# Kernel tuning notes

Measured on AMD Instinct MI355X. Metric: run time of the kernel, lower is better.

## Reference

```python
import jax, jax.numpy as jnp
import numpy as np

N_NODES, N_EDGES, HIDDEN, N_GRAPHS = 100000, 500000, 128, 2048
ATOM_DIM, BOND_DIM, OUT_DIM = 4, 3, 1


def setup_inputs() -> dict:
    key = jax.random.key(0)
    ks = jax.random.split(key, 13)
    s = 0.05  # small init scale to keep relu+scatter depth iterations numerically tame
    return {
        "x": jax.random.normal(ks[0], (N_NODES, ATOM_DIM), jnp.float32),
        "edge_index": jax.random.randint(ks[1], (2, N_EDGES), 0, N_NODES, dtype=jnp.int32),
        "edge_attr": jax.random.normal(ks[2], (N_EDGES, BOND_DIM), jnp.float32),
        "batch": jnp.sort(jax.random.randint(ks[3], (N_NODES,), 0, N_GRAPHS, dtype=jnp.int32)),
        "depth": 3,
        # DMPNN weights (bias=False)
        "W_i": jax.random.normal(ks[4], (HIDDEN, ATOM_DIM + BOND_DIM), jnp.float32) * s,
        "W_m": jax.random.normal(ks[5], (HIDDEN, HIDDEN), jnp.float32) * s,
        "W_a": jax.random.normal(ks[6], (HIDDEN, ATOM_DIM + HIDDEN), jnp.float32) * s,
        # FFN: Linear(d,4d) -> relu -> dropout(eval=identity) -> Linear(4d,d)
        "W1": jax.random.normal(ks[7], (4 * HIDDEN, HIDDEN), jnp.float32) * s,
        "b1": jnp.zeros((4 * HIDDEN,), jnp.float32),
        "W2": jax.random.normal(ks[8], (HIDDEN, 4 * HIDDEN), jnp.float32) * s,
        "b2": jnp.zeros((HIDDEN,), jnp.float32),
        "W_last": jax.random.normal(ks[9], (OUT_DIM, HIDDEN), jnp.float32) * s,
        "b_last": jnp.zeros((OUT_DIM,), jnp.float32),
    }


def reference(x, edge_index, edge_attr, batch, depth, W_i, W_m, W_a, W1, b1, W2, b2, W_last, b_last):
    src, dst = edge_index[0], edge_index[1]
    E = edge_attr.shape[0]
    N = x.shape[0]
    # h: per-edge state [E, H]
    h = jax.nn.relu(jnp.concatenate([x[src], edge_attr], axis=1) @ W_i.T)
    for _ in range(depth):
        # message: relu(W_m h) gathered at src, scatter-add to dst; PyG infers
        # dim_size from h (edge-level here), so aggregation buffer has E rows.
        m = jax.nn.relu(h @ W_m.T)
        h = h + jax.ops.segment_sum(m[src], dst, num_segments=E)
    # index_add_ edge states to nodes
    node_emb = jax.ops.segment_sum(h, dst, num_segments=N)  # [N, H]
    node_emb = jax.nn.relu(jnp.concatenate([x, node_emb], axis=1) @ W_a.T)
    # global_add_pool over graphs
    g = jax.ops.segment_sum(node_emb, batch, num_segments=N_GRAPHS)  # [G, H]
    g = jax.nn.relu(g @ W1.T + b1) @ W2.T + b2  # FFN (dropout eval = identity)
    return g @ W_last.T + b_last  # [G, OUT_DIM]
```

## Files before the change

kernel.cpp:

```cpp
#include <hip/hip_runtime.h>


#define NN 100000
#define NE 500000
#define HID 128
#define NG 2048
#define NB_SCAN 391
#define NBLK128 782

typedef __attribute__((ext_vector_type(8))) short bf16x8;
typedef __attribute__((ext_vector_type(4))) float f32x4;

__device__ __forceinline__ float b2f(ushort u) {
  return __uint_as_float(((uint)u) << 16);
}
__device__ __forceinline__ ushort f2b(float f) {
  uint u = __float_as_uint(f);
  return (ushort)((u + 0x7FFF + ((u >> 16) & 1)) >> 16);
}
__device__ __forceinline__ void acc8(float* a, bf16x8 v) {
#pragma unroll
  for (int j = 0; j < 8; ++j) a[j] += b2f((ushort)v[j]);
}
__device__ __forceinline__ bf16x8 pack8(const float* a) {
  bf16x8 o;
#pragma unroll
  for (int j = 0; j < 8; ++j) o[j] = (short)f2b(a[j]);
  return o;
}
__device__ __forceinline__ size_t taddr(int n, int c8) {
  return ((size_t)(c8 >> 4) * NN + n) * 16 + (c8 & 8);
}

__global__ __launch_bounds__(256) void k_convw(const float* __restrict__ Wm,
    const float* __restrict__ Wa, ushort* __restrict__ wmb, ushort* __restrict__ wab) {
  int i = blockIdx.x * 256 + threadIdx.x;
  if (i >= HID * HID) return;
  wmb[i] = f2b(Wm[i]);
  int c = i >> 7, k = i & 127;
  wab[i] = f2b(Wa[c * 132 + 4 + k]);
}

__global__ __launch_bounds__(256) void k_init_h8(const int* __restrict__ src,
    const float* __restrict__ x, const float* __restrict__ ea,
    const float* __restrict__ Wi, ushort* __restrict__ hT) {
  __shared__ float wis[HID * 7];
  for (int i = threadIdx.x; i < HID * 7; i += 256) wis[i] = Wi[i];
  __syncthreads();
  int idx = blockIdx.x * 256 + threadIdx.x;
  int e = idx >> 4, chunk = idx & 15;
  if (e >= NN) return;
  int s = src[e];
  float4 xv = *reinterpret_cast<const float4*>(&x[(size_t)s * 4]);
  float e0 = ea[(size_t)e*3+0], e1 = ea[(size_t)e*3+1], e2 = ea[(size_t)e*3+2];
  const float* w = &wis[chunk * 56];
  float a[8];
#pragma unroll
  for (int j = 0; j < 8; ++j) {
    const float* wj = &w[j * 7];
    float t = xv.x*wj[0] + xv.y*wj[1] + xv.z*wj[2] + xv.w*wj[3]
            + e0*wj[4] + e1*wj[5] + e2*wj[6];
    a[j] = fmaxf(t, 0.f);
  }
  *reinterpret_cast<bf16x8*>(&hT[((size_t)(chunk >> 1) * NN + e) * 16 + (chunk & 1) * 8]) = pack8(a);
}

__global__ __launch_bounds__(256) void k_hist2(const int* __restrict__ dst,
    int* __restrict__ cnt, int* __restrict__ cnt_lo) {
  int e = blockIdx.x * 256 + threadIdx.x;
  if (e >= NE) return;
  int d = dst[e];
  atomicAdd(&cnt[d], 1);
  if (e < NN) atomicAdd(&cnt_lo[d], 1);
}

__global__ __launch_bounds__(256) void k_scan1(const int* __restrict__ cnt,
    int* __restrict__ outp, int* __restrict__ bsums) {
  __shared__ int s[256];
  int t = threadIdx.x;
  int i = blockIdx.x * 256 + t;
  int v = (i < NN) ? cnt[i] : 0;
  s[t] = v;
  __syncthreads();
  for (int off = 1; off < 256; off <<= 1) {
    int u = (t >= off) ? s[t - off] : 0;
    __syncthreads();
    s[t] += u;
    __syncthreads();
  }
  if (i < NN) outp[i] = s[t] - v;
  if (t == 255) bsums[blockIdx.x] = s[255];
}

__global__ __launch_bounds__(512) void k_scan2(int* __restrict__ bsums) {
  __shared__ int s[512];
  int t = threadIdx.x;
  int v = (t < NB_SCAN) ? bsums[t] : 0;
  s[t] = v;
  __syncthreads();
  for (int off = 1; off < 512; off <<= 1) {
    int u = (t >= off) ? s[t - off] : 0;
    __syncthreads();
    s[t] += u;
    __syncthreads();
  }
  if (t < NB_SCAN) bsums[t] = s[t] - v;
}

__global__ __launch_bounds__(256) void k_scan3(int* __restrict__ outp,
                                               const int* __restrict__ bsums) {
  int i = blockIdx.x * 256 + threadIdx.x;
  if (i < NN) outp[i] += bsums[blockIdx.x];
  if (i == 0) outp[NN] = NE;
}

__global__ __launch_bounds__(256) void k_mid(const int* __restrict__ rowptr,
    const int* __restrict__ cnt_lo, int* __restrict__ midp) {
  int i = blockIdx.x * 256 + threadIdx.x;
  if (i < NN) midp[i] = rowptr[i] + cnt_lo[i];
}

__global__ __launch_bounds__(256) void k_fill2z(const int* __restrict__ src,
    const int* __restrict__ dst, const int* __restrict__ rowptr,
    const int* __restrict__ midp, int* __restrict__ cur_lo,
    int* __restrict__ cur_hi, int* __restrict__ csr_src, int* __restrict__ csr_eid,
    const float* __restrict__ x, const float* __restrict__ ea,
    ushort* __restrict__ zpk) {
  int e = blockIdx.x * 256 + threadIdx.x;
  if (e >= NE) return;
  int d = dst[e];
  int s = src[e];
  int o;
  if (e < NN) {
    o = rowptr[d] + atomicAdd(&cur_lo[d], 1);
    csr_eid[o] = e;
  } else {
    o = midp[d] + atomicAdd(&cur_hi[d], 1);
    float4 xv = *reinterpret_cast<const float4*>(&x[(size_t)s * 4]);
    bf16x8 z;
    z[0] = (short)f2b(xv.x); z[1] = (short)f2b(xv.y);
    z[2] = (short)f2b(xv.z); z[3] = (short)f2b(xv.w);
    z[4] = (short)f2b(ea[(size_t)e*3+0]);
    z[5] = (short)f2b(ea[(size_t)e*3+1]);
    z[6] = (short)f2b(ea[(size_t)e*3+2]);
    z[7] = 0;
    *reinterpret_cast<bf16x8*>(&zpk[(size_t)o * 8]) = z;
  }
  csr_src[o] = s;
}

__global__ __launch_bounds__(256) void k_goff(const int* __restrict__ batch,
                                              int* __restrict__ goff) {
  int g = blockIdx.x * 256 + threadIdx.x;
  if (g > NG) return;
  int lo = 0, hi = NN;
  while (lo < hi) { int mid = (lo + hi) >> 1; if (batch[mid] < g) lo = mid + 1; else hi = mid; }
  goff[g] = lo;
}

template <bool HASX>
__global__ __launch_bounds__(256) void k_mfma(const ushort* __restrict__ A,
    const ushort* __restrict__ Wb, const float* __restrict__ X,
    const float* __restrict__ WaF, ushort* __restrict__ O, int nrows) {
  int tid = threadIdx.x;
  int wave = tid >> 6;
  int lane = tid & 63;
  int wr = wave >> 1, wc = wave & 1;
  int row0 = blockIdx.x * 64 + wr * 32;
  int col0 = wc * 64;
  int l15 = lane & 15, l4 = lane >> 4;

  f32x4 acc[2][4];
#pragma unroll
  for (int mi = 0; mi < 2; ++mi)
#pragma unroll
    for (int ni = 0; ni < 4; ++ni) acc[mi][ni] = (f32x4){0.f, 0.f, 0.f, 0.f};

  if (HASX) {
    float4 wv[4];
#pragma unroll
    for (int ni = 0; ni < 4; ++ni)
      wv[ni] = *reinterpret_cast<const float4*>(&WaF[(size_t)(col0 + ni * 16 + l15) * 132]);
#pragma unroll
    for (int mi = 0; mi < 2; ++mi)
#pragma unroll
      for (int j = 0; j < 4; ++j) {
        int r = row0 + mi * 16 + l4 * 4 + j;
        if (r < nrows) {
          float4 xv = *reinterpret_cast<const float4*>(&X[(size_t)r * 4]);
#pragma unroll
          for (int ni = 0; ni < 4; ++ni)
            acc[mi][ni][j] = xv.x * wv[ni].x + xv.y * wv[ni].y
                           + xv.z * wv[ni].z + xv.w * wv[ni].w;
        }
      }
  }

  const bf16x8 zero8 = {0, 0, 0, 0, 0, 0, 0, 0};
#pragma unroll
  for (int k0 = 0; k0 < HID; k0 += 32) {
    bf16x8 a[2], b[4];
    int c8 = k0 + l4 * 8;
#pragma unroll
    for (int mi = 0; mi < 2; ++mi) {
      int r = row0 + mi * 16 + l15;
      a[mi] = (r < nrows)
            ? *reinterpret_cast<const bf16x8*>(&A[taddr(r, c8)])
            : zero8;
    }
#pragma unroll
    for (int ni = 0; ni < 4; ++ni) {
      int c = col0 + ni * 16 + l15;
      b[ni] = *reinterpret_cast<const bf16x8*>(&Wb[(size_t)c * HID + k0 + l4 * 8]);
    }
#pragma unroll
    for (int mi = 0; mi < 2; ++mi)
#pragma unroll
      for (int ni = 0; ni < 4; ++ni)
        acc[mi][ni] = __builtin_amdgcn_mfma_f32_16x16x32_bf16(a[mi], b[ni], acc[mi][ni], 0, 0, 0);
  }

#pragma unroll
  for (int mi = 0; mi < 2; ++mi)
#pragma unroll
    for (int j = 0; j < 4; ++j) {
      int r = row0 + mi * 16 + l4 * 4 + j;
      if (r >= nrows) continue;
#pragma unroll
      for (int ni = 0; ni < 4; ++ni) {
        int plane = wc * 4 + ni;
        O[((size_t)plane * NN + r) * 16 + l15] = f2b(fmaxf(acc[mi][ni][j], 0.f));
      }
    }
}

__global__ __launch_bounds__(256) void k_gather_x(const ushort* __restrict__ mT,
    const int* __restrict__ rowptr, const int* __restrict__ csr_src,
    ushort* __restrict__ hT) {
  int plane = blockIdx.x & 7;
  int nb = blockIdx.x >> 3;
  int n = nb * 128 + (threadIdx.x >> 1);
  if (n >= NN) return;
  int half8 = (threadIdx.x & 1) * 8;
  size_t pb = (size_t)plane * NN;
  size_t base = (pb + n) * 16 + half8;
  const bf16x8 zero8 = {0, 0, 0, 0, 0, 0, 0, 0};
  float a[8];
  bf16x8 hv = *reinterpret_cast<const bf16x8*>(&hT[base]);
#pragma unroll
  for (int j = 0; j < 8; ++j) a[j] = b2f((ushort)hv[j]);
  int beg = rowptr[n], end = rowptr[n + 1];
  for (int i = beg; i < end; i += 8) {
    bf16x8 v[8];
#pragma unroll
    for (int k = 0; k < 8; ++k) {
      v[k] = zero8;
      if (i + k < end) {
        int s = csr_src[i + k];
        v[k] = *reinterpret_cast<const bf16x8*>(&mT[(pb + s) * 16 + half8]);
      }
    }
#pragma unroll
    for (int k = 0; k < 8; ++k) acc8(a, v[k]);
  }
  *reinterpret_cast<bf16x8*>(&hT[base]) = pack8(a);
}

__global__ __launch_bounds__(256) void k_node_agg_x(const ushort* __restrict__ hT,
    const int* __restrict__ rowptr, const int* __restrict__ midp,
    const int* __restrict__ csr_eid, const ushort* __restrict__ zpk,
    const float* __restrict__ Wi, ushort* __restrict__ neT) {
  int plane = blockIdx.x & 7;
  int nb = blockIdx.x >> 3;
  int n = nb * 128 + (threadIdx.x >> 1);
  if (n >= NN) return;
  int half8 = (threadIdx.x & 1) * 8;
  int c8 = plane * 16 + half8;
  float w[8][7];
#pragma unroll
  for (int j = 0; j < 8; ++j)
#pragma unroll
    for (int k = 0; k < 7; ++k) w[j][k] = Wi[(c8 + j) * 7 + k];
  size_t pb = (size_t)plane * NN;
  int beg = rowptr[n], mid = midp[n], end = rowptr[n + 1];
  const bf16x8 zero8 = {0, 0, 0, 0, 0, 0, 0, 0};
  float a[8];
#pragma unroll
  for (int j = 0; j < 8; ++j) a[j] = 0.f;

  for (int i = beg; i < mid; i += 4) {
    bf16x8 v[4];
#pragma unroll
    for (int k = 0; k < 4; ++k) {
      v[k] = zero8;
      if (i + k < mid) {
        int e = csr_eid[i + k];
        v[k] = *reinterpret_cast<const bf16x8*>(&hT[(pb + e) * 16 + half8]);
      }
    }
#pragma unroll
    for (int k = 0; k < 4; ++k) acc8(a, v[k]);
  }

  for (int i = mid; i < end; i += 4) {
    bf16x8 zv[4];
#pragma unroll
    for (int k = 0; k < 4; ++k) {
      zv[k] = zero8;
      if (i + k < end)
        zv[k] = *reinterpret_cast<const bf16x8*>(&zpk[(size_t)(i + k) * 8]);
    }
#pragma unroll
    for (int k = 0; k < 4; ++k) {
      if (i + k < end) {
        float z0 = b2f((ushort)zv[k][0]), z1 = b2f((ushort)zv[k][1]);
        float z2 = b2f((ushort)zv[k][2]), z3 = b2f((ushort)zv[k][3]);
        float z4 = b2f((ushort)zv[k][4]), z5 = b2f((ushort)zv[k][5]);
        float z6 = b2f((ushort)zv[k][6]);
#pragma unroll
        for (int j = 0; j < 8; ++j) {
          float t = z0*w[j][0] + z1*w[j][1] + z2*w[j][2] + z3*w[j][3]
                  + z4*w[j][4] + z5*w[j][5] + z6*w[j][6];
          a[j] += fmaxf(t, 0.f);
        }
      }
    }
  }
  *reinterpret_cast<bf16x8*>(&neT[(pb + n) * 16 + half8]) = pack8(a);
}

__global__ __launch_bounds__(256) void k_pool(const ushort* __restrict__ na,
    const int* __restrict__ goff, float* __restrict__ g) {
  int idx = blockIdx.x * 256 + threadIdx.x;
  int gid = idx >> 4;
  if (gid >= NG) return;
  int c8 = (idx & 15) * 8;
  size_t pbase = (size_t)(c8 >> 4) * NN;
  int off = c8 & 8;
  int beg = goff[gid], end = goff[gid + 1];
  float a[8];
#pragma unroll
  for (int j = 0; j < 8; ++j) a[j] = 0.f;
  for (int n = beg; n < end; ++n)
    acc8(a, *reinterpret_cast<const bf16x8*>(&na[(pbase + n) * 16 + off]));
  *reinterpret_cast<float4*>(&g[(size_t)gid * HID + c8]) = make_float4(a[0], a[1], a[2], a[3]);
  *reinterpret_cast<float4*>(&g[(size_t)gid * HID + c8 + 4]) = make_float4(a[4], a[5], a[6], a[7]);
}

template <bool RELU>
__global__ __launch_bounds__(256) void k_gemm64(const float* __restrict__ A,
    const float* __restrict__ W, const float* __restrict__ bias,
    float* __restrict__ O, int nrows, int K, int N) {
  __shared__ float As[64][33];
  __shared__ float Bs[32][68];
  int tid = threadIdx.x;
  int row0 = blockIdx.x * 64;
  int col0 = blockIdx.y * 64;
  int tn = tid & 15;
  int tm = tid >> 4;
  float acc[4][4];
#pragma unroll
  for (int i = 0; i < 4; ++i)
#pragma unroll
    for (int j = 0; j < 4; ++j) acc[i][j] = 0.f;

  for (int k0 = 0; k0 < K; k0 += 32) {
    int ar = tid >> 3;
    int ak = (tid & 7) << 2;
#pragma unroll
    for (int rr = 0; rr < 2; ++rr) {
      int r = row0 + ar + rr * 32;
      float4 v = make_float4(0.f, 0.f, 0.f, 0.f);
      if (r < nrows) v = *reinterpret_cast<const float4*>(&A[(size_t)r * K + k0 + ak]);
      As[ar + rr*32][ak+0] = v.x; As[ar + rr*32][ak+1] = v.y;
      As[ar + rr*32][ak+2] = v.z; As[ar + rr*32][ak+3] = v.w;
    }
    int c = tid & 63;
    int kq = tid >> 6;
#pragma unroll
    for (int it = 0; it < 2; ++it) {
      int kk = kq * 4 + it * 16;
      float4 v = *reinterpret_cast<const float4*>(&W[(size_t)(col0 + c) * K + k0 + kk]);
      Bs[kk+0][c] = v.x; Bs[kk+1][c] = v.y; Bs[kk+2][c] = v.z; Bs[kk+3][c] = v.w;
    }
    __syncthreads();
#pragma unroll 8
    for (int k = 0; k < 32; ++k) {
      float av[4];
#pragma unroll
      for (int i = 0; i < 4; ++i) av[i] = As[tm*4 + i][k];
      float4 bv = *reinterpret_cast<const float4*>(&Bs[k][tn*4]);
#pragma unroll
      for (int i = 0; i < 4; ++i) {
        acc[i][0] = fmaf(av[i], bv.x, acc[i][0]);
        acc[i][1] = fmaf(av[i], bv.y, acc[i][1]);
        acc[i][2] = fmaf(av[i], bv.z, acc[i][2]);
        acc[i][3] = fmaf(av[i], bv.w, acc[i][3]);
      }
    }
    __syncthreads();
  }
#pragma unroll
  for (int i = 0; i < 4; ++i) {
    int r = row0 + tm * 4 + i;
    if (r >= nrows) continue;
    float4 o;
    int c = col0 + tn * 4;
    o.x = acc[i][0] + bias[c+0];
    o.y = acc[i][1] + bias[c+1];
    o.z = acc[i][2] + bias[c+2];
    o.w = acc[i][3] + bias[c+3];
    if (RELU) {
      o.x = fmaxf(o.x, 0.f); o.y = fmaxf(o.y, 0.f);
      o.z = fmaxf(o.z, 0.f); o.w = fmaxf(o.w, 0.f);
    }
    *reinterpret_cast<float4*>(&O[(size_t)r * N + c]) = o;
  }
}

__global__ __launch_bounds__(256) void k_last(const float* __restrict__ g3,
    const float* __restrict__ Wl, const float* __restrict__ bl,
    float* __restrict__ out) {
  int wid = (blockIdx.x * 256 + threadIdx.x) >> 6;
  int lane = threadIdx.x & 63;
  if (wid >= NG) return;
  float a = g3[(size_t)wid*128 + lane] * Wl[lane]
          + g3[(size_t)wid*128 + 64 + lane] * Wl[64 + lane];
  for (int off = 32; off; off >>= 1) a += __shfl_down(a, off);
  if (lane == 0) out[wid] = a + bl[0];
}

extern "C" void kernel_launch(void* const* d_in, const int* in_sizes, int n_in,
                              void* d_out, int out_size, void* d_ws, size_t ws_size,
                              hipStream_t stream) {
  const float* x    = (const float*)d_in[0];
  const int*   eidx = (const int*)d_in[1];
  const float* ea   = (const float*)d_in[2];
  const int*   batch= (const int*)d_in[3];
  const float* Wi   = (const float*)d_in[5];
  const float* Wm   = (const float*)d_in[6];
  const float* Wa   = (const float*)d_in[7];
  const float* W1   = (const float*)d_in[8];
  const float* b1   = (const float*)d_in[9];
  const float* W2   = (const float*)d_in[10];
  const float* b2   = (const float*)d_in[11];
  const float* Wl   = (const float*)d_in[12];
  const float* bl   = (const float*)d_in[13];
  float* out = (float*)d_out;

  const int* src = eidx;
  const int* dst = eidx + NE;

  char* p = (char*)d_ws;
  ushort* hb  = (ushort*)p; p += (size_t)NN * HID * 2;
  ushort* mb  = (ushort*)p; p += (size_t)NN * HID * 2;
  ushort* wmb = (ushort*)p; p += (size_t)HID * HID * 2;
  ushort* wab = (ushort*)p; p += (size_t)HID * HID * 2;
  ushort* zpk = (ushort*)p; p += (size_t)NE * 8 * 2;
  float* g  = (float*)p; p += (size_t)NG * 128 * 4;
  float* g2 = (float*)p; p += (size_t)NG * 512 * 4;
  float* g3 = (float*)p; p += (size_t)NG * 128 * 4;
  int* csr_src = (int*)p; p += (size_t)NE * 4;
  int* csr_eid = (int*)p; p += (size_t)NE * 4;
  int* cnt    = (int*)p; p += (size_t)NN * 4;
  int* cnt_lo = (int*)p; p += (size_t)NN * 4;
  int* cur_lo = (int*)p; p += (size_t)NN * 4;
  int* cur_hi = (int*)p; p += (size_t)NN * 4;
  int* rowptr = (int*)p; p += (size_t)(NN + 4) * 4;
  int* midp   = (int*)p; p += (size_t)NN * 4;
  int* bsums  = (int*)p; p += 512 * 4;
  int* goff   = (int*)p; p += (size_t)(NG + 4) * 4;

  hipMemsetAsync(cnt, 0, (size_t)4 * NN * sizeof(int), stream);
  k_hist2<<<(NE + 255) / 256, 256, 0, stream>>>(dst, cnt, cnt_lo);
  k_scan1<<<NB_SCAN, 256, 0, stream>>>(cnt, rowptr, bsums);
  k_scan2<<<1, 512, 0, stream>>>(bsums);
  k_scan3<<<NB_SCAN, 256, 0, stream>>>(rowptr, bsums);
  k_mid  <<<NB_SCAN, 256, 0, stream>>>(rowptr, cnt_lo, midp);
  k_fill2z<<<(NE + 255) / 256, 256, 0, stream>>>(src, dst, rowptr, midp,
                                                 cur_lo, cur_hi, csr_src, csr_eid,
                                                 x, ea, zpk);
  k_goff <<<(NG + 256) / 256, 256, 0, stream>>>(batch, goff);

  k_convw<<<(HID * HID + 255) / 256, 256, 0, stream>>>(Wm, Wa, wmb, wab);

  k_init_h8<<<(NN * 16 + 255) / 256, 256, 0, stream>>>(src, x, ea, Wi, hb);

  int ggrid = (NN + 63) / 64;
  for (int it = 0; it < 3; ++it) {
    k_mfma<false><<<ggrid, 256, 0, stream>>>(hb, wmb, nullptr, nullptr, mb, NN);
    k_gather_x<<<8 * NBLK128, 256, 0, stream>>>(mb, rowptr, csr_src, hb);
  }

  k_node_agg_x<<<8 * NBLK128, 256, 0, stream>>>(hb, rowptr, midp, csr_eid,
                                                zpk, Wi, mb);
  k_mfma<true><<<ggrid, 256, 0, stream>>>(mb, wab, x, Wa, hb, NN);

  k_pool<<<(NG * 16 + 255) / 256, 256, 0, stream>>>(hb, goff, g);

  dim3 grid1((NG + 63) / 64, 512 / 64);
  k_gemm64<true><<<grid1, 256, 0, stream>>>(g, W1, b1, g2, NG, 128, 512);
  dim3 grid2((NG + 63) / 64, 128 / 64);
  k_gemm64<false><<<grid2, 256, 0, stream>>>(g2, W2, b2, g3, NG, 512, 128);
  k_last<<<(NG * 64) / 256, 256, 0, stream>>>(g3, Wl, bl, out);
}
```

Measured before the change: 435.9 us.

## Merge setup kernels and remap gather/node-agg thread-to-work assignment

Folds the midpoint computation into the scan-fixup kernel and merges the weight conversion with the graph-offset search into one launch, removing several small kernel launches. The edge gather now gives each thread a full 16-channel plane row, two 16-byte loads per neighbor, so each index is loaded once per plane instead of twice, at the cost of more registers and fewer threads. Node aggregation maps the 16 channel chunks of a node onto consecutive threads so one node's rowptr/midp reads are shared across a half-wave, while the per-plane hT/neT accesses become strided.

```diff
diff --git a/kernel.cpp b/kernel.cpp
--- a/kernel.cpp
+++ b/kernel.cpp
@@ -6,7 +6,7 @@
 #define HID 128
 #define NG 2048
 #define NB_SCAN 391
-#define NBLK128 782
+#define NBLK256 391
 
 typedef __attribute__((ext_vector_type(8))) short bf16x8;
 typedef __attribute__((ext_vector_type(4))) float f32x4;
@@ -30,15 +30,6 @@
 }
 __device__ __forceinline__ size_t taddr(int n, int c8) {
   return ((size_t)(c8 >> 4) * NN + n) * 16 + (c8 & 8);
-}
-
-__global__ __launch_bounds__(256) void k_convw(const float* __restrict__ Wm,
-    const float* __restrict__ Wa, ushort* __restrict__ wmb, ushort* __restrict__ wab) {
-  int i = blockIdx.x * 256 + threadIdx.x;
-  if (i >= HID * HID) return;
-  wmb[i] = f2b(Wm[i]);
-  int c = i >> 7, k = i & 127;
-  wab[i] = f2b(Wa[c * 132 + 4 + k]);
 }
 
 __global__ __launch_bounds__(256) void k_init_h8(const int* __restrict__ src,
@@ -107,17 +98,16 @@
   if (t < NB_SCAN) bsums[t] = s[t] - v;
 }
 
-__global__ __launch_bounds__(256) void k_scan3(int* __restrict__ outp,
-                                               const int* __restrict__ bsums) {
+__global__ __launch_bounds__(256) void k_scan3m(int* __restrict__ outp,
+    const int* __restrict__ bsums, const int* __restrict__ cnt_lo,
+    int* __restrict__ midp) {
   int i = blockIdx.x * 256 + threadIdx.x;
-  if (i < NN) outp[i] += bsums[blockIdx.x];
+  if (i < NN) {
+    int v = outp[i] + bsums[blockIdx.x];
+    outp[i] = v;
+    midp[i] = v + cnt_lo[i];
+  }
   if (i == 0) outp[NN] = NE;
-}
-
-__global__ __launch_bounds__(256) void k_mid(const int* __restrict__ rowptr,
-    const int* __restrict__ cnt_lo, int* __restrict__ midp) {
-  int i = blockIdx.x * 256 + threadIdx.x;
-  if (i < NN) midp[i] = rowptr[i] + cnt_lo[i];
 }
 
 __global__ __launch_bounds__(256) void k_fill2z(const int* __restrict__ src,
@@ -149,13 +139,23 @@
   csr_src[o] = s;
 }
 
-__global__ __launch_bounds__(256) void k_goff(const int* __restrict__ batch,
-                                              int* __restrict__ goff) {
-  int g = blockIdx.x * 256 + threadIdx.x;
-  if (g > NG) return;
-  int lo = 0, hi = NN;
-  while (lo < hi) { int mid = (lo + hi) >> 1; if (batch[mid] < g) lo = mid + 1; else hi = mid; }
-  goff[g] = lo;
+__global__ __launch_bounds__(256) void k_misc(const float* __restrict__ Wm,
+    const float* __restrict__ Wa, ushort* __restrict__ wmb,
+    ushort* __restrict__ wab, const int* __restrict__ batch,
+    int* __restrict__ goff) {
+  int gb = blockIdx.x;
+  if (gb < 64) {
+    int i = gb * 256 + threadIdx.x;
+    wmb[i] = f2b(Wm[i]);
+    int c = i >> 7, k = i & 127;
+    wab[i] = f2b(Wa[c * 132 + 4 + k]);
+  } else {
+    int g = (gb - 64) * 256 + threadIdx.x;
+    if (g > NG) return;
+    int lo = 0, hi = NN;
+    while (lo < hi) { int mid = (lo + hi) >> 1; if (batch[mid] < g) lo = mid + 1; else hi = mid; }
+    goff[g] = lo;
+  }
 }
 
 template <bool HASX>
@@ -239,48 +239,51 @@
     ushort* __restrict__ hT) {
   int plane = blockIdx.x & 7;
   int nb = blockIdx.x >> 3;
-  int n = nb * 128 + (threadIdx.x >> 1);
+  int n = nb * 256 + threadIdx.x;
   if (n >= NN) return;
-  int half8 = (threadIdx.x & 1) * 8;
   size_t pb = (size_t)plane * NN;
-  size_t base = (pb + n) * 16 + half8;
+  size_t base = (pb + n) * 16;
   const bf16x8 zero8 = {0, 0, 0, 0, 0, 0, 0, 0};
-  float a[8];
-  bf16x8 hv = *reinterpret_cast<const bf16x8*>(&hT[base]);
-#pragma unroll
-  for (int j = 0; j < 8; ++j) a[j] = b2f((ushort)hv[j]);
+  float a[16];
+  bf16x8 h0 = *reinterpret_cast<const bf16x8*>(&hT[base]);
+  bf16x8 h1 = *reinterpret_cast<const bf16x8*>(&hT[base + 8]);
+#pragma unroll
+  for (int j = 0; j < 8; ++j) { a[j] = b2f((ushort)h0[j]); a[8+j] = b2f((ushort)h1[j]); }
   int beg = rowptr[n], end = rowptr[n + 1];
-  for (int i = beg; i < end; i += 8) {
-    bf16x8 v[8];
-#pragma unroll
-    for (int k = 0; k < 8; ++k) {
-      v[k] = zero8;
+  for (int i = beg; i < end; i += 4) {
+    bf16x8 v0[4], v1[4];
+#pragma unroll
+    for (int k = 0; k < 4; ++k) {
+      v0[k] = zero8; v1[k] = zero8;
       if (i + k < end) {
-        int s = csr_src[i + k];
-        v[k] = *reinterpret_cast<const bf16x8*>(&mT[(pb + s) * 16 + half8]);
+        size_t sb = (pb + csr_src[i + k]) * 16;
+        v0[k] = *reinterpret_cast<const bf16x8*>(&mT[sb]);
+        v1[k] = *reinterpret_cast<const bf16x8*>(&mT[sb + 8]);
       }
     }
 #pragma unroll
-    for (int k = 0; k < 8; ++k) acc8(a, v[k]);
+    for (int k = 0; k < 4; ++k) { acc8(a, v0[k]); acc8(a + 8, v1[k]); }
   }
   *reinterpret_cast<bf16x8*>(&hT[base]) = pack8(a);
-}
-
-__global__ __launch_bounds__(256) void k_node_agg_x(const ushort* __restrict__ hT,
+  *reinterpret_cast<bf16x8*>(&hT[base + 8]) = pack8(a + 8);
+}
+
+__global__ __launch_bounds__(256) void k_node_agg3(const ushort* __restrict__ hT,
     const int* __restrict__ rowptr, const int* __restrict__ midp,
     const int* __restrict__ csr_eid, const ushort* __restrict__ zpk,
     const float* __restrict__ Wi, ushort* __restrict__ neT) {
-  int plane = blockIdx.x & 7;
-  int nb = blockIdx.x >> 3;
-  int n = nb * 128 + (threadIdx.x >> 1);
+  int idx = blockIdx.x * 256 + threadIdx.x;
+  int n = idx >> 4;
+  int t = idx & 15;
+  int plane = t >> 1;
+  int half8 = (t & 1) * 8;
+  int c8 = t * 8;
+  float w[8][7];
+#pragma unroll
+  for (int j = 0; j < 8; ++j)
+#pragma unroll
+    for (int k = 0; k < 7; ++k) w[j][k] = Wi[(c8 + j) * 7 + k];
   if (n >= NN) return;
-  int half8 = (threadIdx.x & 1) * 8;
-  int c8 = plane * 16 + half8;
-  float w[8][7];
-#pragma unroll
-  for (int j = 0; j < 8; ++j)
-#pragma unroll
-    for (int k = 0; k < 7; ++k) w[j][k] = Wi[(c8 + j) * 7 + k];
   size_t pb = (size_t)plane * NN;
   int beg = rowptr[n], mid = midp[n], end = rowptr[n + 1];
   const bf16x8 zero8 = {0, 0, 0, 0, 0, 0, 0, 0};
@@ -319,9 +322,9 @@
         float z6 = b2f((ushort)zv[k][6]);
 #pragma unroll
         for (int j = 0; j < 8; ++j) {
-          float t = z0*w[j][0] + z1*w[j][1] + z2*w[j][2] + z3*w[j][3]
-                  + z4*w[j][4] + z5*w[j][5] + z6*w[j][6];
-          a[j] += fmaxf(t, 0.f);
+          float tt = z0*w[j][0] + z1*w[j][1] + z2*w[j][2] + z3*w[j][3]
+                   + z4*w[j][4] + z5*w[j][5] + z6*w[j][6];
+          a[j] += fmaxf(tt, 0.f);
         }
       }
     }
@@ -475,25 +478,22 @@
   k_hist2<<<(NE + 255) / 256, 256, 0, stream>>>(dst, cnt, cnt_lo);
   k_scan1<<<NB_SCAN, 256, 0, stream>>>(cnt, rowptr, bsums);
   k_scan2<<<1, 512, 0, stream>>>(bsums);
-  k_scan3<<<NB_SCAN, 256, 0, stream>>>(rowptr, bsums);
-  k_mid  <<<NB_SCAN, 256, 0, stream>>>(rowptr, cnt_lo, midp);
+  k_scan3m<<<NB_SCAN, 256, 0, stream>>>(rowptr, bsums, cnt_lo, midp);
   k_fill2z<<<(NE + 255) / 256, 256, 0, stream>>>(src, dst, rowptr, midp,
                                                  cur_lo, cur_hi, csr_src, csr_eid,
                                                  x, ea, zpk);
-  k_goff <<<(NG + 256) / 256, 256, 0, stream>>>(batch, goff);
-
-  k_convw<<<(HID * HID + 255) / 256, 256, 0, stream>>>(Wm, Wa, wmb, wab);
+  k_misc<<<64 + 9, 256, 0, stream>>>(Wm, Wa, wmb, wab, batch, goff);
 
   k_init_h8<<<(NN * 16 + 255) / 256, 256, 0, stream>>>(src, x, ea, Wi, hb);
 
   int ggrid = (NN + 63) / 64;
   for (int it = 0; it < 3; ++it) {
     k_mfma<false><<<ggrid, 256, 0, stream>>>(hb, wmb, nullptr, nullptr, mb, NN);
-    k_gather_x<<<8 * NBLK128, 256, 0, stream>>>(mb, rowptr, csr_src, hb);
-  }
-
-  k_node_agg_x<<<8 * NBLK128, 256, 0, stream>>>(hb, rowptr, midp, csr_eid,
-                                                zpk, Wi, mb);
+    k_gather_x<<<8 * NBLK256, 256, 0, stream>>>(mb, rowptr, csr_src, hb);
+  }
+
+  k_node_agg3<<<(NN * 16 + 255) / 256, 256, 0, stream>>>(hb, rowptr, midp,
+                                                         csr_eid, zpk, Wi, mb);
   k_mfma<true><<<ggrid, 256, 0, stream>>>(mb, wab, x, Wa, hb, NN);
 
   k_pool<<<(NG * 16 + 255) / 256, 256, 0, stream>>>(hb, goff, g);
```

New measurement: 439.2 us. About the same (+0.8%).
